# Performance work log

Measured on AMD Instinct MI355X. Metric: run time of the kernel, lower is better.

Reference implementation:

```python
import jax, jax.numpy as jnp
import numpy as np

NUM_HEADS = 8      # in_channels // num_head_channels = 512 // 64
NUM_GROUPS = 32    # GroupNorm groups
EPS = 1e-5


def setup_inputs() -> dict:
    key = jax.random.key(0)
    ks = jax.random.split(key, 6)
    C = 512
    x = jax.random.normal(ks[0], (8, C, 32, 32), dtype=jnp.float32)
    gn_w = jax.random.normal(ks[1], (C,), dtype=jnp.float32) * 0.1 + 1.0
    gn_b = jax.random.normal(ks[2], (C,), dtype=jnp.float32) * 0.1
    qkv_w = jax.random.normal(ks[3], (3 * C, C), dtype=jnp.float32) / np.sqrt(C)
    qkv_b = jnp.zeros((3 * C,), dtype=jnp.float32)
    # NOTE: original zero-initializes to_out; we use small random weights so the
    # attention path contributes to the output (math is identical).
    out_w = jax.random.normal(ks[4], (C, C), dtype=jnp.float32) * 0.02
    out_b = jax.random.normal(ks[5], (C,), dtype=jnp.float32) * 0.02
    return {"x": x, "gn_w": gn_w, "gn_b": gn_b, "qkv_w": qkv_w,
            "qkv_b": qkv_b, "out_w": out_w, "out_b": out_b}


def _group_norm(net, gn_w, gn_b):
    b, c, t = net.shape
    g = net.reshape(b, NUM_GROUPS, c // NUM_GROUPS, t)
    mu = jnp.mean(g, axis=(2, 3), keepdims=True)
    var = jnp.var(g, axis=(2, 3), keepdims=True)
    n = ((g - mu) * jax.lax.rsqrt(var + EPS)).reshape(b, c, t)
    return n * gn_w[None, :, None] + gn_b[None, :, None]


def reference(x, gn_w, gn_b, qkv_w, qkv_b, out_w, out_b):
    b, c, h, w = x.shape
    area = h * w
    inp = x.reshape(b, c, area)                      # [b, c, t]
    n = _group_norm(inp, gn_w, gn_b)
    # 1x1 conv1d == channel GEMM
    qkv = jnp.einsum('oc,bct->bot', qkv_w, n) + qkv_b[None, :, None]  # [b, 3c, t]
    hd = c // NUM_HEADS
    # split_qkv_after_heads: view(b*H, 3*hd, area) then split along channel
    qkv = qkv.reshape(b * NUM_HEADS, 3 * hd, area)
    q, k, v = qkv[:, :hd], qkv[:, hd:2 * hd], qkv[:, 2 * hd:]
    scale = 1.0 / np.sqrt(np.sqrt(hd))               # sqrt-sqrt per-tensor scale
    attn = jnp.einsum('bct,bcs->bts', q * scale, k * scale)  # [bH, t, s]
    prob = jax.nn.softmax(attn, axis=-1)
    net = jnp.einsum('bts,bcs->bct', prob, v).reshape(b, c, area)
    out = jnp.einsum('oc,bct->bot', out_w, net) + out_b[None, :, None]
    return (inp + out).reshape(b, c, h, w)
```

## Files before the change

### kernel.cpp

```cpp
#include <hip/hip_runtime.h>
#include <hip/hip_bf16.h>

typedef __bf16 bf16_t;
typedef __bf16 bf16x8 __attribute__((ext_vector_type(8)));
typedef __bf16 bf16x4 __attribute__((ext_vector_type(4)));
typedef short  s16x4  __attribute__((ext_vector_type(4)));
typedef float  f32x4  __attribute__((ext_vector_type(4)));

#define B_DIM 8
#define C_DIM 512
#define T_DIM 1024
#define NH 8
#define HD 64

#define QSCALE 0.180336880111112f

__device__ __forceinline__ f32x4 mfma16_bf16(bf16x4 a, bf16x4 b, f32x4 c) {
    return __builtin_amdgcn_mfma_f32_16x16x16bf16_1k(
        __builtin_bit_cast(s16x4, a), __builtin_bit_cast(s16x4, b), c, 0, 0, 0);
}

__device__ __forceinline__ void block_sync_lds() {
    asm volatile("s_waitcnt lgkmcnt(0)" ::: "memory");
    __builtin_amdgcn_s_barrier();
}

__global__ __launch_bounds__(256) void prep_w(const float* __restrict__ w1,
                                              const float* __restrict__ w2,
                                              bf16_t* __restrict__ o1,
                                              bf16_t* __restrict__ o2)
{
    int tid = blockIdx.x * 256 + threadIdx.x;
    for (int p = 0; p < 4; ++p) {
        int q = tid + p * 65536;
        const f32x4* src;
        bf16x4* dst;
        int qq;
        if (q < 196608) { src = (const f32x4*)w1; dst = (bf16x4*)o1; qq = q; }
        else            { src = (const f32x4*)w2; dst = (bf16x4*)o2; qq = q - 196608; }
        f32x4 f = src[qq];
        bf16x4 h;
        for (int j = 0; j < 4; ++j) h[j] = (bf16_t)f[j];
        dst[qq] = h;
    }
}

__global__ __launch_bounds__(256) void gn_kernel(const float* __restrict__ x,
                                                 const float* __restrict__ gw,
                                                 const float* __restrict__ gb,
                                                 bf16_t* __restrict__ n_t)
{
    __shared__ bf16_t sX[16384];
    __shared__ float sred[8];
    int tid = threadIdx.x;
    int bb  = blockIdx.x >> 5;
    int g   = blockIdx.x & 31;
    const f32x4* xg4 = reinterpret_cast<const f32x4*>(x + (size_t)(bb * C_DIM + g * 16) * T_DIM);

    float s = 0.f, sq = 0.f;
    for (int i = 0; i < 16; ++i) {
        int v = tid + i * 256;
        f32x4 f = xg4[v];
        bf16x4 h;
        for (int j = 0; j < 4; ++j) {
            s += f[j]; sq += f[j] * f[j];
            h[j] = (bf16_t)f[j];
        }
        *reinterpret_cast<bf16x4*>(sX + v * 4) = h;
    }
    for (int off = 1; off < 64; off <<= 1) {
        s  += __shfl_xor(s, off);
        sq += __shfl_xor(sq, off);
    }
    int wv = tid >> 6;
    if ((tid & 63) == 0) { sred[wv * 2] = s; sred[wv * 2 + 1] = sq; }
    __syncthreads();
    s  = sred[0] + sred[2] + sred[4] + sred[6];
    sq = sred[1] + sred[3] + sred[5] + sred[7];
    float mean = s * (1.f / 16384.f);
    float var  = sq * (1.f / 16384.f) - mean * mean;
    float rs   = rsqrtf(var + 1e-5f);

    int hf = tid & 1;
    float aa[8], bbias[8];
    for (int j = 0; j < 8; ++j) {
        int c = hf * 8 + j;
        float av = gw[g * 16 + c] * rs;
        aa[j] = av;
        bbias[j] = gb[g * 16 + c] - mean * av;
    }
    bf16_t* ob = n_t + (size_t)bb * T_DIM * C_DIM + g * 16 + hf * 8;
    for (int p = 0; p < 8; ++p) {
        int t = (tid >> 1) + p * 128;
        bf16x8 o;
        for (int j = 0; j < 8; ++j) {
            float xv = (float)sX[(hf * 8 + j) * 1024 + t];
            o[j] = (bf16_t)(xv * aa[j] + bbias[j]);
        }
        *reinterpret_cast<bf16x8*>(ob + (size_t)t * C_DIM) = o;
    }
}

__global__ __launch_bounds__(256, 4) void qkv_gemm_kernel(
    const bf16_t* __restrict__ wqb, const float* __restrict__ bq,
    const bf16_t* __restrict__ n_t, bf16_t* __restrict__ qkv)
{
    __shared__ bf16_t sA[128 * 72];
    __shared__ bf16_t sB[128 * 72];
    int tid = threadIdx.x;
    int w = tid >> 6, lane = tid & 63, quad = lane >> 4, l15 = lane & 15;
    int bx = blockIdx.x;
    int t0 = blockIdx.y * 128;
    int bb = blockIdx.z;
    int o0 = bx * 128;
    const bf16_t* Ab = wqb + (size_t)o0 * C_DIM;
    const bf16_t* Bb = n_t + ((size_t)bb * T_DIM + t0) * C_DIM;

    f32x4 acc[4][4];
    for (int mt = 0; mt < 4; ++mt)
        for (int nt = 0; nt < 4; ++nt)
            acc[mt][nt] = f32x4{0.f, 0.f, 0.f, 0.f};
    int mw0 = (w >> 1) * 64;
    int nw0 = (w & 1) * 64;

    for (int k0 = 0; k0 < C_DIM; k0 += 64) {
        for (int i = 0; i < 4; ++i) {
            int v = tid + i * 256;
            int row = v >> 3, c8 = v & 7;
            *reinterpret_cast<bf16x8*>(sA + row * 72 + c8 * 8) =
                *reinterpret_cast<const bf16x8*>(Ab + (size_t)row * C_DIM + k0 + c8 * 8);
        }
        for (int i = 0; i < 4; ++i) {
            int v = tid + i * 256;
            int row = v >> 3, c8 = v & 7;
            *reinterpret_cast<bf16x8*>(sB + row * 72 + c8 * 8) =
                *reinterpret_cast<const bf16x8*>(Bb + (size_t)row * C_DIM + k0 + c8 * 8);
        }
        __syncthreads();
        for (int kk = 0; kk < 2; ++kk) {
            bf16x8 af[4], bfr[4];
            for (int mt = 0; mt < 4; ++mt)
                af[mt] = *reinterpret_cast<const bf16x8*>(sA + (mw0 + mt * 16 + l15) * 72 + kk * 32 + quad * 8);
            for (int nt = 0; nt < 4; ++nt)
                bfr[nt] = *reinterpret_cast<const bf16x8*>(sB + (nw0 + nt * 16 + l15) * 72 + kk * 32 + quad * 8);
            for (int mt = 0; mt < 4; ++mt)
                for (int nt = 0; nt < 4; ++nt)
                    acc[mt][nt] = __builtin_amdgcn_mfma_f32_16x16x32_bf16(af[mt], bfr[nt], acc[mt][nt], 0, 0, 0);
        }
        __syncthreads();
    }

    for (int half = 0; half < 2; ++half) {
        int chunk = bx * 2 + half;
        int h = chunk / 3, type = chunk % 3;
        size_t base = ((size_t)(bb * NH + h) * 3 + type) * (64 * 1024);
        bool mine = (mw0 >> 6) == half;

        if (type < 2) {
            float scl = (type == 0) ? QSCALE : 1.0f;
            if (mine)
                for (int mt = 0; mt < 4; ++mt)
                    for (int nt = 0; nt < 4; ++nt)
                        for (int r = 0; r < 4; ++r) {
                            int mw = mt * 16 + quad * 4 + r;
                            int tl = nw0 + nt * 16 + l15;
                            float v = (acc[mt][nt][r] + bq[o0 + half * 64 + mw]) * scl;
                            sB[tl * 72 + mw] = (bf16_t)v;
                        }
            __syncthreads();
            for (int i = 0; i < 4; ++i) {
                int v = tid + i * 256;
                int tl = v >> 3, c8 = v & 7;
                bf16x8 d = *reinterpret_cast<const bf16x8*>(sB + tl * 72 + c8 * 8);
                *reinterpret_cast<bf16x8*>(qkv + base + (size_t)(t0 + tl) * 64 + c8 * 8) = d;
            }
            __syncthreads();
        } else {
            if (mine)
                for (int mt = 0; mt < 4; ++mt)
                    for (int nt = 0; nt < 4; ++nt)
                        for (int r = 0; r < 4; ++r) {
                            int mw = mt * 16 + quad * 4 + r;
                            int tl = nw0 + nt * 16 + l15;
                            float v = acc[mt][nt][r] + bq[o0 + half * 64 + mw];
                            sB[mw * 136 + tl] = (bf16_t)v;
                        }
            __syncthreads();
            for (int i = 0; i < 4; ++i) {
                int v = tid + i * 256;
                int cc = v >> 4, t8 = (v & 15) * 8;
                bf16x8 d = *reinterpret_cast<const bf16x8*>(sB + cc * 136 + t8);
                *reinterpret_cast<bf16x8*>(qkv + base + (size_t)cc * 1024 + t0 + t8) = d;
            }
            __syncthreads();
        }
    }
}

__global__ __launch_bounds__(256, 2) void attn_kernel(const bf16_t* __restrict__ qkv,
                                                      bf16_t* __restrict__ net_t)
{
    __shared__ bf16_t sK0[64 * 72];
    __shared__ bf16_t sV0[64 * 72];
    __shared__ bf16_t sK1[64 * 72];
    __shared__ bf16_t sV1[64 * 72];
    int tid = threadIdx.x;
    int w = tid >> 6, lane = tid & 63, quad = lane >> 4, l15 = lane & 15;
    int bh = blockIdx.x;
    int qt = blockIdx.y;
    size_t qb = (size_t)bh * 3 * 65536;
    const bf16_t* Qg = qkv + qb + (size_t)qt * 8192;
    const bf16_t* Kg = qkv + qb + 65536;
    const bf16_t* Vg = qkv + qb + 2 * 65536;

    bf16x8 qf[2][2];
    for (int tt = 0; tt < 2; ++tt)
        for (int kk = 0; kk < 2; ++kk)
            qf[tt][kk] = *reinterpret_cast<const bf16x8*>(
                Qg + (size_t)(tt * 64 + w * 16 + l15) * 64 + kk * 32 + quad * 8);

    int vrow = tid >> 3;
    int vcol = (tid & 7) * 8;

    bf16x8 kA[2], vA[2], kB[2], vB[2];

    auto load_tiles = [&](bf16x8* kr, bf16x8* vr, int s0) {
        for (int i = 0; i < 2; ++i) {
            int r = vrow + i * 32;
            kr[i] = *reinterpret_cast<const bf16x8*>(Kg + (size_t)(s0 + r) * 64 + vcol);
            vr[i] = *reinterpret_cast<const bf16x8*>(Vg + (size_t)r * 1024 + s0 + vcol);
        }
    };
    auto write_tiles = [&](bf16_t* sKb, bf16_t* sVb, const bf16x8* kr, const bf16x8* vr) {
        for (int i = 0; i < 2; ++i) {
            int r = vrow + i * 32;
            *reinterpret_cast<bf16x8*>(sKb + r * 72 + vcol) = kr[i];
            *reinterpret_cast<bf16x8*>(sVb + r * 72 + vcol) = vr[i];
        }
    };

    f32x4 O0[4], O1[4];
    for (int i = 0; i < 4; ++i) {
        O0[i] = f32x4{0.f, 0.f, 0.f, 0.f};
        O1[i] = f32x4{0.f, 0.f, 0.f, 0.f};
    }
    f32x4 L0 = f32x4{0.f, 0.f, 0.f, 0.f};
    f32x4 L1 = f32x4{0.f, 0.f, 0.f, 0.f};
    const bf16x4 kONES = bf16x4{(bf16_t)1.f, (bf16_t)1.f, (bf16_t)1.f, (bf16_t)1.f};

    auto compute_tile = [&](const bf16_t* sKb, const bf16_t* sVb) {
        __builtin_amdgcn_s_setprio(1);
        for (int mt = 0; mt < 4; ++mt) {
            const bf16_t* krow = sKb + (mt * 16 + l15) * 72 + quad * 8;
            bf16x8 kf0 = *reinterpret_cast<const bf16x8*>(krow);
            bf16x8 kf1 = *reinterpret_cast<const bf16x8*>(krow + 32);
            f32x4 S0 = f32x4{0.f, 0.f, 0.f, 0.f};
            f32x4 S1 = f32x4{0.f, 0.f, 0.f, 0.f};
            S0 = __builtin_amdgcn_mfma_f32_16x16x32_bf16(kf0, qf[0][0], S0, 0, 0, 0);
            S1 = __builtin_amdgcn_mfma_f32_16x16x32_bf16(kf0, qf[1][0], S1, 0, 0, 0);
            S0 = __builtin_amdgcn_mfma_f32_16x16x32_bf16(kf1, qf[0][1], S0, 0, 0, 0);
            S1 = __builtin_amdgcn_mfma_f32_16x16x32_bf16(kf1, qf[1][1], S1, 0, 0, 0);
            bf16x4 pf0, pf1;
            for (int r = 0; r < 4; ++r) {
                pf0[r] = (bf16_t)__builtin_amdgcn_exp2f(S0[r]);
                pf1[r] = (bf16_t)__builtin_amdgcn_exp2f(S1[r]);
            }
            L0 = mfma16_bf16(kONES, pf0, L0);
            L1 = mfma16_bf16(kONES, pf1, L1);
            for (int ct = 0; ct < 4; ++ct) {
                bf16x4 vf = *reinterpret_cast<const bf16x4*>(sVb + (ct * 16 + l15) * 72 + mt * 16 + quad * 4);
                O0[ct] = mfma16_bf16(vf, pf0, O0[ct]);
                O1[ct] = mfma16_bf16(vf, pf1, O1[ct]);
            }
        }
        __builtin_amdgcn_s_setprio(0);
    };

    load_tiles(kA, vA, 0);
    write_tiles(sK0, sV0, kA, vA);
    load_tiles(kB, vB, 64);
    block_sync_lds();

    for (int st2 = 0; st2 < 8; ++st2) {
        write_tiles(sK1, sV1, kB, vB);
        if (st2 < 7) load_tiles(kA, vA, (2 * st2 + 2) * 64);
        compute_tile(sK0, sV0);
        block_sync_lds();
        if (st2 < 7) {
            write_tiles(sK0, sV0, kA, vA);
            load_tiles(kB, vB, (2 * st2 + 3) * 64);
        }
        compute_tile(sK1, sV1);
        if (st2 < 7) block_sync_lds();
    }

    float inv0 = 1.f / L0[0];
    float inv1 = 1.f / L1[0];

    int bb = bh >> 3, h = bh & 7;
    int tbase = qt * 128 + w * 16 + l15;
    bf16_t* orow0 = net_t + ((size_t)bb * T_DIM + tbase) * C_DIM + h * 64;
    bf16_t* orow1 = net_t + ((size_t)bb * T_DIM + tbase + 64) * C_DIM + h * 64;
    for (int ct = 0; ct < 4; ++ct) {
        bf16x4 o4, o5;
        for (int r = 0; r < 4; ++r) {
            o4[r] = (bf16_t)(O0[ct][r] * inv0);
            o5[r] = (bf16_t)(O1[ct][r] * inv1);
        }
        *reinterpret_cast<bf16x4*>(orow0 + ct * 16 + quad * 4) = o4;
        *reinterpret_cast<bf16x4*>(orow1 + ct * 16 + quad * 4) = o5;
    }
}

__global__ __launch_bounds__(256) void out_gemm_kernel(
    const bf16_t* __restrict__ wob, const float* __restrict__ bo,
    const bf16_t* __restrict__ net_t, const float* __restrict__ x,
    float* __restrict__ out)
{
    __shared__ bf16_t sA[64 * 72];
    __shared__ bf16_t sB[128 * 72];
    int tid = threadIdx.x;
    int w = tid >> 6, lane = tid & 63, quad = lane >> 4, l15 = lane & 15;
    int o0 = blockIdx.x * 64;
    int t0 = blockIdx.y * 128;
    int bb = blockIdx.z;
    const bf16_t* Ab = wob + (size_t)o0 * C_DIM;
    const bf16_t* Bb = net_t + ((size_t)bb * T_DIM + t0) * C_DIM;

    f32x4 acc[2][4];
    for (int mt = 0; mt < 2; ++mt)
        for (int nt = 0; nt < 4; ++nt)
            acc[mt][nt] = f32x4{0.f, 0.f, 0.f, 0.f};
    int mw0 = (w >> 1) * 32;
    int nw0 = (w & 1) * 64;

    for (int k0 = 0; k0 < C_DIM; k0 += 64) {
        for (int i = 0; i < 2; ++i) {
            int v = tid + i * 256;
            int row = v >> 3, c8 = v & 7;
            *reinterpret_cast<bf16x8*>(sA + row * 72 + c8 * 8) =
                *reinterpret_cast<const bf16x8*>(Ab + (size_t)row * C_DIM + k0 + c8 * 8);
        }
        for (int i = 0; i < 4; ++i) {
            int v = tid + i * 256;
            int row = v >> 3, c8 = v & 7;
            *reinterpret_cast<bf16x8*>(sB + row * 72 + c8 * 8) =
                *reinterpret_cast<const bf16x8*>(Bb + (size_t)row * C_DIM + k0 + c8 * 8);
        }
        __syncthreads();
        for (int kk = 0; kk < 2; ++kk) {
            bf16x8 af[2], bfr[4];
            for (int mt = 0; mt < 2; ++mt)
                af[mt] = *reinterpret_cast<const bf16x8*>(sA + (mw0 + mt * 16 + l15) * 72 + kk * 32 + quad * 8);
            for (int nt = 0; nt < 4; ++nt)
                bfr[nt] = *reinterpret_cast<const bf16x8*>(sB + (nw0 + nt * 16 + l15) * 72 + kk * 32 + quad * 8);
            for (int mt = 0; mt < 2; ++mt)
                for (int nt = 0; nt < 4; ++nt)
                    acc[mt][nt] = __builtin_amdgcn_mfma_f32_16x16x32_bf16(af[mt], bfr[nt], acc[mt][nt], 0, 0, 0);
        }
        __syncthreads();
    }

    for (int mt = 0; mt < 2; ++mt)
        for (int nt = 0; nt < 4; ++nt)
            for (int r = 0; r < 4; ++r) {
                int o = o0 + mw0 + mt * 16 + quad * 4 + r;
                int t = t0 + nw0 + nt * 16 + l15;
                size_t idx = ((size_t)bb * C_DIM + o) * T_DIM + t;
                out[idx] = acc[mt][nt][r] + bo[o] + x[idx];
            }
}

extern "C" void kernel_launch(void* const* d_in, const int* in_sizes, int n_in,
                              void* d_out, int out_size, void* d_ws, size_t ws_size,
                              hipStream_t stream)
{
    const float* x     = (const float*)d_in[0];
    const float* gn_w  = (const float*)d_in[1];
    const float* gn_b  = (const float*)d_in[2];
    const float* qkv_w = (const float*)d_in[3];
    const float* qkv_b = (const float*)d_in[4];
    const float* out_w = (const float*)d_in[5];
    const float* out_b = (const float*)d_in[6];
    float* out = (float*)d_out;

    char* ws = (char*)d_ws;
    bf16_t* n_t   = (bf16_t*)(ws);
    bf16_t* qkv   = (bf16_t*)(ws + 8388608);
    bf16_t* net_t = (bf16_t*)(ws + 33554432);
    bf16_t* wqb   = (bf16_t*)(ws + 41943040);
    bf16_t* wob   = (bf16_t*)(ws + 41943040 + 1572864);

    prep_w<<<dim3(256), 256, 0, stream>>>(qkv_w, out_w, wqb, wob);
    gn_kernel<<<dim3(256), 256, 0, stream>>>(x, gn_w, gn_b, n_t);
    qkv_gemm_kernel<<<dim3(12, 8, 8), 256, 0, stream>>>(wqb, qkv_b, n_t, qkv);
    attn_kernel<<<dim3(64, 8), 256, 0, stream>>>(qkv, net_t);
    out_gemm_kernel<<<dim3(8, 8, 8), 256, 0, stream>>>(wob, out_b, net_t, x, out);
}
```

Baseline: 152.9 us.

## Fuse weight conversion into groupnorm launch and deepen attention K/V pipeline

The fp32-to-bf16 weight conversion moves into extra blocks of the groupnorm kernel, which removes one kernel launch. The attention kernel changes from two LDS K/V buffers to four and processes two tiles per barrier phase. This halves the number of barriers and keeps more global loads in flight per step. The cost is double the LDS footprint, about 73KB per block, which may lower occupancy below the two blocks per CU requested in launch bounds, plus more registers held for prefetched tiles.

```diff
diff --git a/kernel.cpp b/kernel.cpp
--- a/kernel.cpp
+++ b/kernel.cpp
@@ -25,34 +25,36 @@
     __builtin_amdgcn_s_barrier();
 }
 
-__global__ __launch_bounds__(256) void prep_w(const float* __restrict__ w1,
-                                              const float* __restrict__ w2,
-                                              bf16_t* __restrict__ o1,
-                                              bf16_t* __restrict__ o2)
-{
-    int tid = blockIdx.x * 256 + threadIdx.x;
-    for (int p = 0; p < 4; ++p) {
-        int q = tid + p * 65536;
-        const f32x4* src;
-        bf16x4* dst;
-        int qq;
-        if (q < 196608) { src = (const f32x4*)w1; dst = (bf16x4*)o1; qq = q; }
-        else            { src = (const f32x4*)w2; dst = (bf16x4*)o2; qq = q - 196608; }
-        f32x4 f = src[qq];
-        bf16x4 h;
-        for (int j = 0; j < 4; ++j) h[j] = (bf16_t)f[j];
-        dst[qq] = h;
-    }
-}
-
 __global__ __launch_bounds__(256) void gn_kernel(const float* __restrict__ x,
                                                  const float* __restrict__ gw,
                                                  const float* __restrict__ gb,
-                                                 bf16_t* __restrict__ n_t)
+                                                 bf16_t* __restrict__ n_t,
+                                                 const float* __restrict__ w1,
+                                                 const float* __restrict__ w2,
+                                                 bf16_t* __restrict__ o1,
+                                                 bf16_t* __restrict__ o2)
 {
     __shared__ bf16_t sX[16384];
     __shared__ float sred[8];
     int tid = threadIdx.x;
+
+    if (blockIdx.x >= 256) {
+        int tid2 = (blockIdx.x - 256) * 256 + tid;
+        for (int p = 0; p < 16; ++p) {
+            int q = tid2 + p * 16384;
+            const f32x4* src;
+            bf16x4* dst;
+            int qq;
+            if (q < 196608) { src = (const f32x4*)w1; dst = (bf16x4*)o1; qq = q; }
+            else            { src = (const f32x4*)w2; dst = (bf16x4*)o2; qq = q - 196608; }
+            f32x4 f = src[qq];
+            bf16x4 h;
+            for (int j = 0; j < 4; ++j) h[j] = (bf16_t)f[j];
+            dst[qq] = h;
+        }
+        return;
+    }
+
     int bb  = blockIdx.x >> 5;
     int g   = blockIdx.x & 31;
     const f32x4* xg4 = reinterpret_cast<const f32x4*>(x + (size_t)(bb * C_DIM + g * 16) * T_DIM);
@@ -200,10 +202,8 @@
 __global__ __launch_bounds__(256, 2) void attn_kernel(const bf16_t* __restrict__ qkv,
                                                       bf16_t* __restrict__ net_t)
 {
-    __shared__ bf16_t sK0[64 * 72];
-    __shared__ bf16_t sV0[64 * 72];
-    __shared__ bf16_t sK1[64 * 72];
-    __shared__ bf16_t sV1[64 * 72];
+    __shared__ bf16_t sK[4][64 * 72];
+    __shared__ bf16_t sV[4][64 * 72];
     int tid = threadIdx.x;
     int w = tid >> 6, lane = tid & 63, quad = lane >> 4, l15 = lane & 15;
     int bh = blockIdx.x;
@@ -277,21 +277,32 @@
     };
 
     load_tiles(kA, vA, 0);
-    write_tiles(sK0, sV0, kA, vA);
     load_tiles(kB, vB, 64);
+    write_tiles(sK[0], sV[0], kA, vA);
+    write_tiles(sK[1], sV[1], kB, vB);
+    load_tiles(kA, vA, 128);
+    load_tiles(kB, vB, 192);
     block_sync_lds();
 
-    for (int st2 = 0; st2 < 8; ++st2) {
-        write_tiles(sK1, sV1, kB, vB);
-        if (st2 < 7) load_tiles(kA, vA, (2 * st2 + 2) * 64);
-        compute_tile(sK0, sV0);
+    for (int ep = 0; ep < 4; ++ep) {
+        write_tiles(sK[2], sV[2], kA, vA);
+        write_tiles(sK[3], sV[3], kB, vB);
+        if (ep < 3) {
+            load_tiles(kA, vA, (4 * ep + 4) * 64);
+            load_tiles(kB, vB, (4 * ep + 5) * 64);
+        }
+        compute_tile(sK[0], sV[0]);
+        compute_tile(sK[1], sV[1]);
         block_sync_lds();
-        if (st2 < 7) {
-            write_tiles(sK0, sV0, kA, vA);
-            load_tiles(kB, vB, (2 * st2 + 3) * 64);
-        }
-        compute_tile(sK1, sV1);
-        if (st2 < 7) block_sync_lds();
+        if (ep < 3) {
+            write_tiles(sK[0], sV[0], kA, vA);
+            write_tiles(sK[1], sV[1], kB, vB);
+            load_tiles(kA, vA, (4 * ep + 6) * 64);
+            load_tiles(kB, vB, (4 * ep + 7) * 64);
+        }
+        compute_tile(sK[2], sV[2]);
+        compute_tile(sK[3], sV[3]);
+        if (ep < 3) block_sync_lds();
     }
 
     float inv0 = 1.f / L0[0];
@@ -391,8 +402,7 @@
     bf16_t* wqb   = (bf16_t*)(ws + 41943040);
     bf16_t* wob   = (bf16_t*)(ws + 41943040 + 1572864);
 
-    prep_w<<<dim3(256), 256, 0, stream>>>(qkv_w, out_w, wqb, wob);
-    gn_kernel<<<dim3(256), 256, 0, stream>>>(x, gn_w, gn_b, n_t);
+    gn_kernel<<<dim3(320), 256, 0, stream>>>(x, gn_w, gn_b, n_t, qkv_w, out_w, wqb, wob);
     qkv_gemm_kernel<<<dim3(12, 8, 8), 256, 0, stream>>>(wqb, qkv_b, n_t, qkv);
     attn_kernel<<<dim3(64, 8), 256, 0, stream>>>(qkv, net_t);
     out_gemm_kernel<<<dim3(8, 8, 8), 256, 0, stream>>>(wob, out_b, net_t, x, out);
```

Result: faster. 149.7 us (-2.1%).
